# Performance work log

Hardware: AMD Instinct MI355X
Metric: run time of the kernel (lower is better)

Reference implementation:

```python
import jax, jax.numpy as jnp
import numpy as np

N = 20000   # nodes
E = 320000  # edges
T = 12      # sequence_length
H = 64      # hidden_dim
CIN = 16    # input_dim_per_step
L = 3       # num_st_layers
BN_EPS = 1e-5


def setup_inputs() -> dict:
    key = jax.random.key(0)
    ks = jax.random.split(key, 30)
    s = 0.05
    rn = lambda k, shp: jax.random.normal(k, shp, jnp.float32) * s
    inp = {
        "x": jax.random.normal(ks[0], (N, T * CIN), jnp.float32),
        "edge_index": jax.random.randint(ks[1], (2, E), 0, N, jnp.int32),
        # embedding
        "We": rn(ks[2], (CIN, H)), "be": rn(ks[3], (H,)),
        # stacked per-layer params for the 3 ST layers
        "gcn_W": rn(ks[4], (L, H, H)), "gcn_b": rn(ks[5], (L, H)),
        "conv_w": rn(ks[6], (L, H, H, 3)), "conv_b": rn(ks[7], (L, H)),
        "bn_g": jnp.ones((L, H), jnp.float32), "bn_b": rn(ks[8], (L, H)),
        "bn_m": rn(ks[9], (L, H)),
        "bn_v": jax.random.uniform(ks[10], (L, H), jnp.float32, 0.5, 1.5),
        # temporal attention MLP (H -> H//2 -> 1)
        "ta_w1": rn(ks[11], (H, H // 2)), "ta_b1": rn(ks[12], (H // 2,)),
        "ta_w2": rn(ks[13], (H // 2, 1)), "ta_b2": rn(ks[14], (1,)),
        # feature attention MLP (T -> T//2 -> 1)
        "fa_w1": rn(ks[15], (T, T // 2)), "fa_b1": rn(ks[16], (T // 2,)),
        "fa_w2": rn(ks[17], (T // 2, 1)), "fa_b2": rn(ks[18], (1,)),
        # output MLP (H -> H//2 -> 1)
        "ow1": rn(ks[19], (H, H // 2)), "ob1": rn(ks[20], (H // 2,)),
        "ow2": rn(ks[21], (H // 2, 1)), "ob2": rn(ks[22], (1,)),
    }
    return inp


def reference(x, edge_index, We, be, gcn_W, gcn_b, conv_w, conv_b,
              bn_g, bn_b, bn_m, bn_v, ta_w1, ta_b1, ta_w2, ta_b2,
              fa_w1, fa_b1, fa_w2, fa_b2, ow1, ob1, ow2, ob2):
    n = x.shape[0]
    # --- GCN normalization with self-loops (PyG gcn_norm) ---
    loops = jnp.arange(n, dtype=edge_index.dtype)
    src = jnp.concatenate([edge_index[0], loops])
    dst = jnp.concatenate([edge_index[1], loops])
    deg = jax.ops.segment_sum(jnp.ones_like(src, jnp.float32), dst, num_segments=n)
    dinv = 1.0 / jnp.sqrt(deg)  # deg >= 1 thanks to self-loops
    coef = dinv[src] * dinv[dst]  # [E+N]

    # --- per-timestep embedding (vectorized over t) ---
    xr = x.reshape(n, T, CIN)
    emb = jax.nn.relu(jnp.einsum('ntc,ch->nth', xr, We) + be)  # [N,T,H]
    x_st = emb.reshape(n, T * H)

    # --- ST layers (replicating original row-major .view layout mixing) ---
    for i in range(L):
        xi = x_st.reshape(n, H, T)  # [N,C,T]
        # GCNConv per timestep, batched over t: linear then normalized aggregate
        h = jnp.einsum('nct,cd->ndt', xi, gcn_W[i])          # [N,H,T]
        msg = coef[:, None, None] * h[src]                   # [E+N,H,T]
        agg = jax.ops.segment_sum(msg, dst, num_segments=n) + gcn_b[i][None, :, None]
        # temporal conv (kernel 3, pad 1) over T
        tmp = jax.lax.conv_general_dilated(
            agg, conv_w[i], (1,), [(1, 1)],
            dimension_numbers=('NCH', 'OIH', 'NCH')) + conv_b[i][None, :, None]
        # BatchNorm1d (eval mode: running stats)
        normed = (tmp - bn_m[i][None, :, None]) / jnp.sqrt(bn_v[i][None, :, None] + BN_EPS)
        normed = normed * bn_g[i][None, :, None] + bn_b[i][None, :, None]
        # residual is Identity (in_channels == out_channels)
        x_st = jax.nn.relu(normed + xi).reshape(n, H * T)

    # --- dual attention pooling ---
    xa = x_st.reshape(n, T, H)
    tw = (jnp.einsum('ntm,mk->ntk', jax.nn.relu(jnp.einsum('nth,hm->ntm', xa, ta_w1) + ta_b1), ta_w2) + ta_b2)[..., 0]
    tw = jax.nn.softmax(tw, axis=1)                          # [N,T]
    xt = (xa * tw[..., None]).transpose(0, 2, 1)             # [N,H,T]
    fw = (jnp.einsum('nhm,mk->nhk', jax.nn.relu(jnp.einsum('nht,tm->nhm', xt, fa_w1) + fa_b1), fa_w2) + fa_b2)[..., 0]
    fw = jax.nn.softmax(fw, axis=1)                          # [N,H]
    x_final = jnp.sum(xt * fw[..., None], axis=2)            # [N,H]

    # --- output MLP (dropout is identity in eval) ---
    out = jax.nn.relu(x_final @ ow1 + ob1) @ ow2 + ob2       # [N,1]
    return out
```

## Files before the change

### kernel.cpp

```cpp
#include <hip/hip_runtime.h>
#include <cstddef>
#include <cstdint>

#define T_ 12
#define H_ 64
#define CIN_ 16
#define F_ 768
#define BN_EPS 1e-5f
#define RPITCH 88
#define SLOTS 64

typedef float v2f __attribute__((ext_vector_type(2)));
typedef short s8v __attribute__((ext_vector_type(8)));
typedef float f4v __attribute__((ext_vector_type(4)));

__device__ __forceinline__ unsigned short f2bf(float f) {
    unsigned u = __float_as_uint(f);
    unsigned r = (u + 0x7FFFu + ((u >> 16) & 1u)) >> 16;
    return (unsigned short)r;
}
__device__ __forceinline__ float bf2f(unsigned short h) {
    return __uint_as_float(((unsigned)h) << 16);
}
__device__ __forceinline__ v2f bf2x2(unsigned u) {
    v2f r;
    r.x = __uint_as_float(u << 16);
    r.y = __uint_as_float(u & 0xFFFF0000u);
    return r;
}
__device__ __forceinline__ v2f pkfma(v2f a, v2f b, v2f c) {
    return __builtin_elementwise_fma(a, b, c);
}


__global__ void k_init(int* __restrict__ cursor, int n) {
    int i = blockIdx.x * 256 + threadIdx.x;
    if (i < n) cursor[i] = 0;
}


__global__ __launch_bounds__(256) void k_fused(
        const float* __restrict__ gcn_W, const float* __restrict__ gcn_b,
        const float* __restrict__ conv_w,
        unsigned short* __restrict__ wkA, float* __restrict__ bkp,
        const int* __restrict__ srcv, const int* __restrict__ dstv,
        int* __restrict__ cursor, int* __restrict__ csr_src, int e,
        const float* __restrict__ x, const float* __restrict__ We,
        const float* __restrict__ be, unsigned short* __restrict__ xbf, int nT,
        int nbE) {
    __shared__ float smem[5312];
    int b = blockIdx.x;
    int tid = threadIdx.x;

    if (b < 36) {
        int l = b / 12, k = (b / 4) % 3, cq = b & 3;
        const float* Wg = gcn_W + (size_t)l * 4096;
        const float* cw = conv_w + (size_t)l * 12288;
        float* scwT = smem;
        float* sWg  = smem + 4224;
        float* sgb  = smem + 5248;
        for (int i = tid; i < 4096; i += 256)
            scwT[(i & 63) * 66 + (i >> 6)] = cw[(size_t)i * 3 + k];
        for (int i = tid; i < 1024; i += 256)
            sWg[i] = Wg[cq * 16 * 64 + i];
        if (tid < 64) sgb[tid] = gcn_b[(size_t)l * 64 + tid];
        __syncthreads();
#pragma unroll
        for (int j = 0; j < 4; j++) {
            int idx = j * 256 + tid;
            int cc = idx >> 6;
            int o  = idx & 63;
            float acc = 0.f;
            for (int d = 0; d < 64; d++)
                acc += sWg[cc * 64 + d] * scwT[d * 66 + o];
            int cful = cq * 16 + cc;
            int kidx = k * 64 + cful;
            int ks = kidx >> 5, r = kidx & 31;
            int ln = (r >> 3) * 16 + (o & 15);
            int jj = r & 7;
            wkA[((((size_t)l * 24) + (o >> 4) * 6 + ks) * 64 + ln) * 8 + jj] =
                f2bf(acc);
        }
        if (cq == 0 && tid < 64) {
            int o = tid;
            float acc = 0.f;
            for (int d = 0; d < 64; d++)
                acc += sgb[d] * scwT[d * 66 + o];
            bkp[((size_t)l * 3 + k) * 64 + o] = acc;
        }
        return;
    }
    if (b < 36 + nbE) {
        int i = (b - 36) * 256 + tid;
        if (i < e) {
            int d = dstv[i], s = srcv[i];
            int pos = atomicAdd(&cursor[d], 1);
            if (pos < SLOTS) csr_src[d * SLOTS + pos] = s;
        }
        return;
    }
    float* sW = smem;
    float* sb = smem + 1024;
    for (int i = tid; i < CIN_ * H_; i += 256) sW[i] = We[i];
    if (tid < H_) sb[tid] = be[tid];
    __syncthreads();
    int h4  = tid & 15;
    int ntl = tid >> 4;
    int nt  = (b - 36 - nbE) * 16 + ntl;
    if (nt >= nT) return;
    const float4* xp = (const float4*)(x + (size_t)nt * CIN_);
    float4 xv4[4];
    xv4[0] = xp[0]; xv4[1] = xp[1]; xv4[2] = xp[2]; xv4[3] = xp[3];
    const float* xs = (const float*)xv4;
    float acc[4];
#pragma unroll
    for (int j = 0; j < 4; j++) acc[j] = sb[h4 * 4 + j];
#pragma unroll
    for (int c = 0; c < CIN_; c++) {
        float4 w = *(const float4*)&sW[c * H_ + h4 * 4];
        float xc = xs[c];
        acc[0] += xc * w.x; acc[1] += xc * w.y;
        acc[2] += xc * w.z; acc[3] += xc * w.w;
    }
    ushort4 h;
    h.x = f2bf(fmaxf(acc[0], 0.f)); h.y = f2bf(fmaxf(acc[1], 0.f));
    h.z = f2bf(fmaxf(acc[2], 0.f)); h.w = f2bf(fmaxf(acc[3], 0.f));
    *(ushort4*)&xbf[(size_t)nt * H_ + h4 * 4] = h;
}


__global__ __launch_bounds__(256) void k_post(
        const int* __restrict__ cursor, const int* __restrict__ csr_src,
        int2* __restrict__ pack, float* __restrict__ dinv, int n) {
    int i = blockIdx.x * 256 + threadIdx.x;
    int node = i >> 6, slot = i & 63;
    if (node >= n) return;
    int deg = cursor[node];
    float dn = rsqrtf((float)(deg + 1));
    if (slot == 0) dinv[node] = dn;
    if (slot < min(deg, SLOTS)) {
        int s = csr_src[node * SLOTS + slot];
        float cf = rsqrtf((float)(cursor[s] + 1)) * dn;
        pack[node * SLOTS + slot] = make_int2(s * 384, __float_as_int(cf));
    }
}


__global__ __launch_bounds__(256, 8) void k_gather(
        const unsigned short* __restrict__ xin,
        unsigned short* __restrict__ agg,
        const int* __restrict__ degv, const int2* __restrict__ pack,
        const float* __restrict__ dinv, int n) {
    __shared__ int2 sed[4 * SLOTS];
    int b = blockIdx.x;
    int sl = b & 7;
    int g = b >> 3;
    int wave = threadIdx.x >> 6, lane = threadIdx.x & 63;
    int node = g * 4 + wave;
    if (node >= n) return;
    int cnt = min(degv[node], SLOTS);
    if (lane < cnt) sed[wave * SLOTS + lane] = pack[node * SLOTS + lane];
    int lb = sl * 48 + (lane < 48 ? lane : 47);
    const unsigned* xu = (const unsigned*)xin;
    float dn = dinv[node];
    float cs = dn * dn;
    v2f cs2 = {cs, cs};
    v2f acc = bf2x2(xu[node * 384 + lb]) * cs2;
    const int2* sp = &sed[wave * SLOTS];
    int e = 0;
    for (; e + 3 < cnt; e += 4) {
        int2 p0 = sp[e], p1 = sp[e + 1], p2 = sp[e + 2], p3 = sp[e + 3];
        unsigned u0 = xu[p0.x + lb];
        unsigned u1 = xu[p1.x + lb];
        unsigned u2 = xu[p2.x + lb];
        unsigned u3 = xu[p3.x + lb];
        v2f c0 = {__int_as_float(p0.y), __int_as_float(p0.y)};
        v2f c1 = {__int_as_float(p1.y), __int_as_float(p1.y)};
        v2f c2 = {__int_as_float(p2.y), __int_as_float(p2.y)};
        v2f c3 = {__int_as_float(p3.y), __int_as_float(p3.y)};
        acc = pkfma(bf2x2(u0), c0, acc);
        acc = pkfma(bf2x2(u1), c1, acc);
        acc = pkfma(bf2x2(u2), c2, acc);
        acc = pkfma(bf2x2(u3), c3, acc);
    }
    for (; e < cnt; e++) {
        int2 p0 = sp[e];
        unsigned u0 = xu[p0.x + lb];
        v2f c0 = {__int_as_float(p0.y), __int_as_float(p0.y)};
        acc = pkfma(bf2x2(u0), c0, acc);
    }
    if (lane < 48) {
        unsigned o = (unsigned)f2bf(acc.x) | ((unsigned)f2bf(acc.y) << 16);
        ((unsigned*)agg)[node * 384 + lb] = o;
    }
}


#define CONV_CORE()                                                            \
    int tid = threadIdx.x;                                                     \
    int n0 = blockIdx.x * 8;                                                   \
    int wave = tid >> 6, lane = tid & 63;                                      \
    for (int i = tid; i < 8 * 2 * RPITCH; i += 256) {                          \
        int s = i / (2 * RPITCH);                                              \
        int r = i - s * (2 * RPITCH);                                          \
        int row = (r < RPITCH) ? 0 : 13;                                       \
        int c = (r < RPITCH) ? r : r - RPITCH;                                 \
        sxb[s * 14 * RPITCH + row * RPITCH + c] = 0;                           \
    }                                                                          \
    {                                                                          \
        int i0 = 3 * lane;                                                     \
        for (int si = 0; si < 2; si++) {                                       \
            int s = wave * 2 + si;                                             \
            int nn = n0 + s; if (nn >= n) nn = n - 1;                          \
            const uint2* ap = (const uint2*)(agg + (size_t)nn * F_);           \
            uint2 u0 = ap[i0], u1 = ap[i0 + 1], u2 = ap[i0 + 2];               \
            unsigned short* wp = &sxb[s * 14 * RPITCH + RPITCH + lane];        \
            wp[0]           = (unsigned short)u0.x;                            \
            wp[RPITCH]      = (unsigned short)(u0.x >> 16);                    \
            wp[2 * RPITCH]  = (unsigned short)u0.y;                            \
            wp[3 * RPITCH]  = (unsigned short)(u0.y >> 16);                    \
            wp[4 * RPITCH]  = (unsigned short)u1.x;                            \
            wp[5 * RPITCH]  = (unsigned short)(u1.x >> 16);                    \
            wp[6 * RPITCH]  = (unsigned short)u1.y;                            \
            wp[7 * RPITCH]  = (unsigned short)(u1.y >> 16);                    \
            wp[8 * RPITCH]  = (unsigned short)u2.x;                            \
            wp[9 * RPITCH]  = (unsigned short)(u2.x >> 16);                    \
            wp[10 * RPITCH] = (unsigned short)u2.y;                            \
            wp[11 * RPITCH] = (unsigned short)(u2.y >> 16);                    \
        }                                                                      \
    }                                                                          \
    __syncthreads();                                                           \
    int mt = wave;                                                             \
    int q = lane >> 4;                                                         \
    int l15 = lane & 15;                                                       \
    s8v afr[6];                                                                \
    const s8v* Ap = (const s8v*)wkA;                                           \
    for (int ks = 0; ks < 6; ks++) afr[ks] = Ap[(mt * 6 + ks) * 64 + lane];    \
    int obase = mt * 16 + q * 4;                                               \
    float scl[4], shf[4], ball[4], bk0a[4], bk2a[4];                           \
    for (int r = 0; r < 4; r++) {                                              \
        int o = obase + r;                                                     \
        float sc = bng[o] * rsqrtf(bnv[o] + BN_EPS);                           \
        scl[r] = sc;                                                           \
        shf[r] = bnb[o] - bnm[o] * sc;                                         \
        float b0 = bkp[o], b1 = bkp[64 + o], b2 = bkp[128 + o];                \
        ball[r] = cb[o] + b0 + b1 + b2;                                        \
        bk0a[r] = b0; bk2a[r] = b2;                                            \
    }                                                                          \
    f4v accv[6];                                                               \
    for (int nt = 0; nt < 6; nt++) {                                           \
        int nidx = nt * 16 + l15;                                              \
        int s = nidx / 12, t = nidx - 12 * s;                                  \
        const s8v* bp = (const s8v*)&sxb[s * 14 * RPITCH + t * RPITCH + q * 8];\
        f4v acc = {0.f, 0.f, 0.f, 0.f};                                        \
        acc = __builtin_amdgcn_mfma_f32_16x16x32_bf16(afr[0], bp[0],  acc, 0, 0, 0); \
        acc = __builtin_amdgcn_mfma_f32_16x16x32_bf16(afr[1], bp[4],  acc, 0, 0, 0); \
        acc = __builtin_amdgcn_mfma_f32_16x16x32_bf16(afr[2], bp[11], acc, 0, 0, 0); \
        acc = __builtin_amdgcn_mfma_f32_16x16x32_bf16(afr[3], bp[15], acc, 0, 0, 0); \
        acc = __builtin_amdgcn_mfma_f32_16x16x32_bf16(afr[4], bp[22], acc, 0, 0, 0); \
        acc = __builtin_amdgcn_mfma_f32_16x16x32_bf16(afr[5], bp[26], acc, 0, 0, 0); \
        accv[nt] = acc;                                                        \
    }                                                                          \
    __syncthreads();                                                           \
    for (int nt = 0; nt < 6; nt++) {                                           \
        int nidx = nt * 16 + l15;                                              \
        int s = nidx / 12, t = nidx - 12 * s;                                  \
        unsigned short* dp = &sxb[s * F_ + t];                                 \
        for (int r = 0; r < 4; r++) {                                          \
            float bias = ball[r];                                              \
            if (t == 0)  bias -= bk0a[r];                                      \
            if (t == 11) bias -= bk2a[r];                                      \
            float v = (accv[nt][r] + bias) * scl[r] + shf[r];                  \
            dp[(obase + r) * 12] = f2bf(v);                                    \
        }                                                                      \
    }                                                                          \
    __syncthreads();


__global__ __launch_bounds__(256, 8) void k_conv(
        const unsigned short* __restrict__ agg,
        const unsigned short* __restrict__ xin,
        unsigned short* __restrict__ xout,
        const unsigned short* __restrict__ wkA,
        const float* __restrict__ bkp, const float* __restrict__ cb,
        const float* __restrict__ bng, const float* __restrict__ bnb,
        const float* __restrict__ bnm, const float* __restrict__ bnv,
        int n) {
    __shared__ __align__(16) unsigned short sxb[8 * 14 * RPITCH];
    CONV_CORE()

#pragma unroll
    for (int cidx = 0; cidx < 3; cidx++) {
        int c = cidx * 256 + tid;
        int s = c / 96, off = c - s * 96;
        int nn = n0 + s;
        if (nn >= n) continue;
        uint4 dv = *(const uint4*)&sxb[s * F_ + off * 8];
        uint4 rv = ((const uint4*)(xin + (size_t)nn * F_))[off];
        uint4 ov;
        unsigned* dvp = (unsigned*)&dv;
        unsigned* rvp = (unsigned*)&rv;
        unsigned* ovp = (unsigned*)&ov;
#pragma unroll
        for (int w = 0; w < 4; w++) {
            v2f d2 = bf2x2(dvp[w]);
            v2f r2 = bf2x2(rvp[w]);
            float lo = fmaxf(d2.x + r2.x, 0.f);
            float hi = fmaxf(d2.y + r2.y, 0.f);
            ovp[w] = (unsigned)f2bf(lo) | ((unsigned)f2bf(hi) << 16);
        }
        *(uint4*)(xout + (size_t)nn * F_ + off * 8) = ov;
    }
}


__global__ __launch_bounds__(256, 7) void k_conv_attn(
        const unsigned short* __restrict__ agg,
        const unsigned short* __restrict__ xin,
        const unsigned short* __restrict__ wkA,
        const float* __restrict__ bkp, const float* __restrict__ cb,
        const float* __restrict__ bng, const float* __restrict__ bnb,
        const float* __restrict__ bnm, const float* __restrict__ bnv,
        const float* __restrict__ taw1, const float* __restrict__ tab1,
        const float* __restrict__ taw2, const float* __restrict__ tab2,
        const float* __restrict__ faw1, const float* __restrict__ fab1,
        const float* __restrict__ faw2, const float* __restrict__ fab2,
        const float* __restrict__ ow1, const float* __restrict__ ob1,
        const float* __restrict__ ow2, const float* __restrict__ ob2,
        float* __restrict__ out, int n) {
    __shared__ __align__(16) unsigned short sxb[8 * 14 * RPITCH];
    __shared__ float sft[96 + 520];
    CONV_CORE()

#pragma unroll
    for (int cidx = 0; cidx < 3; cidx++) {
        int c = cidx * 256 + tid;
        int s = c / 96, off = c - s * 96;
        int nn = n0 + s; if (nn >= n) nn = n - 1;
        uint4 dv = *(const uint4*)&sxb[s * F_ + off * 8];
        uint4 rv = ((const uint4*)(xin + (size_t)nn * F_))[off];
        unsigned* dvp = (unsigned*)&dv;
        unsigned* rvp = (unsigned*)&rv;
#pragma unroll
        for (int w = 0; w < 4; w++) {
            v2f d2 = bf2x2(dvp[w]);
            v2f r2 = bf2x2(rvp[w]);
            float lo = fmaxf(d2.x + r2.x, 0.f);
            float hi = fmaxf(d2.y + r2.y, 0.f);
            dvp[w] = (unsigned)f2bf(lo) | ((unsigned)f2bf(hi) << 16);
        }
        *(uint4*)&sxb[s * F_ + off * 8] = dv;
    }
    __syncthreads();

    float* s_tw = sft;
    float* s_xf = sft + 96;

    {
        int s2 = tid >> 5, m = tid & 31;
        float bm = tab1[m];
        v2f aa0 = {bm, bm}, aa1 = aa0, aa2 = aa0;
        v2f aa3 = aa0, aa4 = aa0, aa5 = aa0;
        const unsigned short* xr = &sxb[s2 * F_];
        float tb2 = tab2[0];
        for (int hh = 0; hh < 64; hh++) {
            const uint2* xp2 = (const uint2*)&xr[hh * 12];
            uint2 w0 = xp2[0], w1 = xp2[1], w2 = xp2[2];
            float wv = taw1[hh * 32 + m];
            v2f wv2 = {wv, wv};
            aa0 = pkfma(bf2x2(w0.x), wv2, aa0);
            aa1 = pkfma(bf2x2(w0.y), wv2, aa1);
            aa2 = pkfma(bf2x2(w1.x), wv2, aa2);
            aa3 = pkfma(bf2x2(w1.y), wv2, aa3);
            aa4 = pkfma(bf2x2(w2.x), wv2, aa4);
            aa5 = pkfma(bf2x2(w2.y), wv2, aa5);
        }
        float w2v = taw2[m];
        float av[12] = {aa0.x, aa0.y, aa1.x, aa1.y, aa2.x, aa2.y,
                        aa3.x, aa3.y, aa4.x, aa4.y, aa5.x, aa5.y};
#pragma unroll
        for (int t = 0; t < 12; t++) {
            float p = fmaxf(av[t], 0.f) * w2v;
            p += __shfl_xor(p, 1); p += __shfl_xor(p, 2);
            p += __shfl_xor(p, 4); p += __shfl_xor(p, 8);
            p += __shfl_xor(p, 16);
            if (m == 0) s_tw[s2 * 12 + t] = p + tb2;
        }
    }
    __syncthreads();

    {
        float fb2 = fab2[0];
        for (int qi = 0; qi < 2; qi++) {
            int ss = wave * 2 + qi;
            float tw[12];
#pragma unroll
            for (int t = 0; t < 12; t++) tw[t] = s_tw[ss * 12 + t];
            float mx = tw[0];
#pragma unroll
            for (int t = 1; t < 12; t++) mx = fmaxf(mx, tw[t]);
            float sum = 0.f;
#pragma unroll
            for (int t = 0; t < 12; t++) { tw[t] = __expf(tw[t] - mx); sum += tw[t]; }
            float inv = 1.f / sum;
            const uint2* xp2 = (const uint2*)&sxb[ss * F_ + lane * 12];
            uint2 w0 = xp2[0], w1 = xp2[1], w2 = xp2[2];
            v2f x0 = bf2x2(w0.x), x1 = bf2x2(w0.y), x2 = bf2x2(w1.x);
            v2f x3 = bf2x2(w1.y), x4 = bf2x2(w2.x), x5 = bf2x2(w2.y);
            float xv[12] = {x0.x, x0.y, x1.x, x1.y, x2.x, x2.y,
                            x3.x, x3.y, x4.x, x4.y, x5.x, x5.y};
            float xt[12];
#pragma unroll
            for (int t = 0; t < 12; t++) xt[t] = xv[t] * tw[t] * inv;
            float lf = fb2;
#pragma unroll
            for (int mm = 0; mm < 6; mm++) {
                float v = fab1[mm];
#pragma unroll
                for (int t = 0; t < 12; t++) v += xt[t] * faw1[t * 6 + mm];
                lf += fmaxf(v, 0.f) * faw2[mm];
            }
            float m2v = lf;
#pragma unroll
            for (int off = 32; off >= 1; off >>= 1)
                m2v = fmaxf(m2v, __shfl_xor(m2v, off));
            float ev = __expf(lf - m2v);
            float sev = ev;
#pragma unroll
            for (int off = 32; off >= 1; off >>= 1) sev += __shfl_xor(sev, off);
            float fwv = ev / sev;
            float xs = 0.f;
#pragma unroll
            for (int t = 0; t < 12; t++) xs += xt[t];
            s_xf[ss * 65 + lane] = fwv * xs;
        }
    }
    __syncthreads();

    {
        int s2 = tid >> 5, m = tid & 31;
        float v = ob1[m];
        const float* xfp = &s_xf[s2 * 65];
        for (int hh = 0; hh < 64; hh++) v += xfp[hh] * ow1[hh * 32 + m];
        float p = fmaxf(v, 0.f) * ow2[m];
        p += __shfl_xor(p, 1); p += __shfl_xor(p, 2);
        p += __shfl_xor(p, 4); p += __shfl_xor(p, 8);
        p += __shfl_xor(p, 16);
        if (m == 0 && n0 + s2 < n) out[n0 + s2] = p + ob2[0];
    }
}


extern "C" void kernel_launch(void* const* d_in, const int* in_sizes, int n_in,
                              void* d_out, int out_size, void* d_ws, size_t ws_size,
                              hipStream_t stream) {
    const float* x      = (const float*)d_in[0];
    const int*   ei     = (const int*)d_in[1];
    const float* We     = (const float*)d_in[2];
    const float* be     = (const float*)d_in[3];
    const float* gcn_W  = (const float*)d_in[4];
    const float* gcn_b  = (const float*)d_in[5];
    const float* conv_w = (const float*)d_in[6];
    const float* conv_b = (const float*)d_in[7];
    const float* bn_g   = (const float*)d_in[8];
    const float* bn_b   = (const float*)d_in[9];
    const float* bn_m   = (const float*)d_in[10];
    const float* bn_v   = (const float*)d_in[11];
    const float* ta_w1  = (const float*)d_in[12];
    const float* ta_b1  = (const float*)d_in[13];
    const float* ta_w2  = (const float*)d_in[14];
    const float* ta_b2  = (const float*)d_in[15];
    const float* fa_w1  = (const float*)d_in[16];
    const float* fa_b1  = (const float*)d_in[17];
    const float* fa_w2  = (const float*)d_in[18];
    const float* fa_b2  = (const float*)d_in[19];
    const float* ow1    = (const float*)d_in[20];
    const float* ob1    = (const float*)d_in[21];
    const float* ow2    = (const float*)d_in[22];
    const float* ob2    = (const float*)d_in[23];

    int n = in_sizes[0] / (T_ * CIN_);
    int e = in_sizes[1] / 2;
    const int* srcv = ei;
    const int* dstv = ei + e;

    char* p = (char*)d_ws;
    auto take = [&](size_t bytes) -> void* {
        void* r = (void*)p;
        p += (bytes + 255) & ~(size_t)255;
        return r;
    };
    int*   cursor    = (int*)take((size_t)n * 4);
    float* dinv      = (float*)take((size_t)n * 4);
    int*   csr_src   = (int*)take((size_t)n * SLOTS * 4);
    int2*  pack      = (int2*)take((size_t)n * SLOTS * 8);
    float* bkp       = (float*)take((size_t)3 * 3 * 64 * 4);
    unsigned short* wkA  = (unsigned short*)take((size_t)3 * 24 * 64 * 8 * 2);
    unsigned short* xabf = (unsigned short*)take((size_t)n * F_ * 2);
    unsigned short* xbbf = (unsigned short*)take((size_t)n * F_ * 2);
    unsigned short* aggb = (unsigned short*)take((size_t)n * F_ * 2);

    int nb_n = (n + 255) / 256;
    int nb_e = (e + 255) / 256;
    int nb8  = (n + 7) / 8;
    int nbG  = 8 * ((n + 3) / 4);
    int nT   = n * T_;
    int nbM  = (nT + 15) / 16;

    k_init<<<nb_n, 256, 0, stream>>>(cursor, n);
    k_fused<<<36 + nb_e + nbM, 256, 0, stream>>>(
        gcn_W, gcn_b, conv_w, wkA, bkp,
        srcv, dstv, cursor, csr_src, e,
        x, We, be, xabf, nT, nb_e);
    k_post<<<(n * SLOTS + 255) / 256, 256, 0, stream>>>(
        cursor, csr_src, pack, dinv, n);

    k_gather<<<nbG, 256, 0, stream>>>(xabf, aggb, cursor, pack, dinv, n);
    k_conv<<<nb8, 256, 0, stream>>>(aggb, xabf, xbbf, wkA, bkp, conv_b,
                                    bn_g, bn_b, bn_m, bn_v, n);
    k_gather<<<nbG, 256, 0, stream>>>(xbbf, aggb, cursor, pack, dinv, n);
    k_conv<<<nb8, 256, 0, stream>>>(aggb, xbbf, xabf,
                                    wkA + (size_t)1 * 24 * 64 * 8,
                                    bkp + (size_t)1 * 3 * 64,
                                    conv_b + (size_t)1 * H_,
                                    bn_g + (size_t)1 * H_, bn_b + (size_t)1 * H_,
                                    bn_m + (size_t)1 * H_, bn_v + (size_t)1 * H_,
                                    n);
    k_gather<<<nbG, 256, 0, stream>>>(xabf, aggb, cursor, pack, dinv, n);
    k_conv_attn<<<nb8, 256, 0, stream>>>(aggb, xabf,
                                         wkA + (size_t)2 * 24 * 64 * 8,
                                         bkp + (size_t)2 * 3 * 64,
                                         conv_b + (size_t)2 * H_,
                                         bn_g + (size_t)2 * H_, bn_b + (size_t)2 * H_,
                                         bn_m + (size_t)2 * H_, bn_v + (size_t)2 * H_,
                                         ta_w1, ta_b1, ta_w2, ta_b2,
                                         fa_w1, fa_b1, fa_w2, fa_b2,
                                         ow1, ob1, ow2, ob2, (float*)d_out, n);
}
```

Measured before the change: 495.0 us.

## Store node features in 8 feature-sliced planes for cache-local gathers

Changes the bf16 activation layout from node-major [N,768] to eight planes of [N,96], one per gather slice, so each k_gather block's random neighbour reads stay within a plane of about 3.8MB instead of spanning the whole 30MB array. The embedding writer, gather, conv input load and residual/output paths are all re-indexed to match the new layout. The gather also uses nontemporal loads for edge packs and nontemporal stores for the aggregate so they do not displace feature data in cache. The conv kernels now read and write with strided per-plane addressing, which costs some coalescing there.

```diff
diff --git a/kernel.cpp b/kernel.cpp
--- a/kernel.cpp
+++ b/kernel.cpp
@@ -9,6 +9,7 @@
 #define BN_EPS 1e-5f
 #define RPITCH 88
 #define SLOTS 64
+
 
 typedef float v2f __attribute__((ext_vector_type(2)));
 typedef short s8v __attribute__((ext_vector_type(8)));
@@ -47,7 +48,7 @@
         int* __restrict__ cursor, int* __restrict__ csr_src, int e,
         const float* __restrict__ x, const float* __restrict__ We,
         const float* __restrict__ be, unsigned short* __restrict__ xbf, int nT,
-        int nbE) {
+        int nbE, int n) {
     __shared__ float smem[5312];
     int b = blockIdx.x;
     int tid = threadIdx.x;
@@ -125,7 +126,10 @@
     ushort4 h;
     h.x = f2bf(fmaxf(acc[0], 0.f)); h.y = f2bf(fmaxf(acc[1], 0.f));
     h.z = f2bf(fmaxf(acc[2], 0.f)); h.w = f2bf(fmaxf(acc[3], 0.f));
-    *(ushort4*)&xbf[(size_t)nt * H_ + h4 * 4] = h;
+    int node = nt / 12, tt = nt - node * 12;
+    int flat = tt * 64 + h4 * 4;
+    int s = flat / 96, rem = flat - s * 96;
+    *(ushort4*)&xbf[((size_t)s * n + node) * 96 + rem] = h;
 }
 
 
@@ -141,7 +145,7 @@
     if (slot < min(deg, SLOTS)) {
         int s = csr_src[node * SLOTS + slot];
         float cf = rsqrtf((float)(cursor[s] + 1)) * dn;
-        pack[node * SLOTS + slot] = make_int2(s * 384, __float_as_int(cf));
+        pack[node * SLOTS + slot] = make_int2(s * 48, __float_as_int(cf));
     }
 }
 
@@ -159,13 +163,18 @@
     int node = g * 4 + wave;
     if (node >= n) return;
     int cnt = min(degv[node], SLOTS);
-    if (lane < cnt) sed[wave * SLOTS + lane] = pack[node * SLOTS + lane];
-    int lb = sl * 48 + (lane < 48 ? lane : 47);
-    const unsigned* xu = (const unsigned*)xin;
+    if (lane < cnt) {
+        long long v = __builtin_nontemporal_load(
+            (const long long*)&pack[node * SLOTS + lane]);
+        sed[wave * SLOTS + lane] = *(int2*)&v;
+    }
+    int planeU = sl * (n * 48);
+    const unsigned* xu = (const unsigned*)xin + planeU;
+    int lb = (lane < 48 ? lane : 47);
     float dn = dinv[node];
     float cs = dn * dn;
     v2f cs2 = {cs, cs};
-    v2f acc = bf2x2(xu[node * 384 + lb]) * cs2;
+    v2f acc = bf2x2(xu[node * 48 + lb]) * cs2;
     const int2* sp = &sed[wave * SLOTS];
     int e = 0;
     for (; e + 3 < cnt; e += 4) {
@@ -191,7 +200,8 @@
     }
     if (lane < 48) {
         unsigned o = (unsigned)f2bf(acc.x) | ((unsigned)f2bf(acc.y) << 16);
-        ((unsigned*)agg)[node * 384 + lb] = o;
+        unsigned* au = (unsigned*)agg + planeU;
+        __builtin_nontemporal_store(o, &au[node * 48 + lane]);
     }
 }
 
@@ -208,12 +218,13 @@
         sxb[s * 14 * RPITCH + row * RPITCH + c] = 0;                           \
     }                                                                          \
     {                                                                          \
-        int i0 = 3 * lane;                                                     \
+        const uint2* ab = (const uint2*)agg;                                   \
+        int pofs = (lane >> 3) * (n * 24) + (lane & 7) * 3;                    \
         for (int si = 0; si < 2; si++) {                                       \
             int s = wave * 2 + si;                                             \
             int nn = n0 + s; if (nn >= n) nn = n - 1;                          \
-            const uint2* ap = (const uint2*)(agg + (size_t)nn * F_);           \
-            uint2 u0 = ap[i0], u1 = ap[i0 + 1], u2 = ap[i0 + 2];               \
+            const uint2* ap = ab + pofs + nn * 24;                             \
+            uint2 u0 = ap[0], u1 = ap[1], u2 = ap[2];                          \
             unsigned short* wp = &sxb[s * 14 * RPITCH + RPITCH + lane];        \
             wp[0]           = (unsigned short)u0.x;                            \
             wp[RPITCH]      = (unsigned short)(u0.x >> 16);                    \
@@ -295,8 +306,10 @@
         int s = c / 96, off = c - s * 96;
         int nn = n0 + s;
         if (nn >= n) continue;
+        int sp = off / 12, rem = off - sp * 12;
+        int gidx = sp * (n * 12) + nn * 12 + rem;
         uint4 dv = *(const uint4*)&sxb[s * F_ + off * 8];
-        uint4 rv = ((const uint4*)(xin + (size_t)nn * F_))[off];
+        uint4 rv = ((const uint4*)xin)[gidx];
         uint4 ov;
         unsigned* dvp = (unsigned*)&dv;
         unsigned* rvp = (unsigned*)&rv;
@@ -309,7 +322,7 @@
             float hi = fmaxf(d2.y + r2.y, 0.f);
             ovp[w] = (unsigned)f2bf(lo) | ((unsigned)f2bf(hi) << 16);
         }
-        *(uint4*)(xout + (size_t)nn * F_ + off * 8) = ov;
+        ((uint4*)xout)[gidx] = ov;
     }
 }
 
@@ -337,8 +350,10 @@
         int c = cidx * 256 + tid;
         int s = c / 96, off = c - s * 96;
         int nn = n0 + s; if (nn >= n) nn = n - 1;
+        int sp = off / 12, rem = off - sp * 12;
+        int gidx = sp * (n * 12) + nn * 12 + rem;
         uint4 dv = *(const uint4*)&sxb[s * F_ + off * 8];
-        uint4 rv = ((const uint4*)(xin + (size_t)nn * F_))[off];
+        uint4 rv = ((const uint4*)xin)[gidx];
         unsigned* dvp = (unsigned*)&dv;
         unsigned* rvp = (unsigned*)&rv;
 #pragma unroll
@@ -511,7 +526,7 @@
     k_fused<<<36 + nb_e + nbM, 256, 0, stream>>>(
         gcn_W, gcn_b, conv_w, wkA, bkp,
         srcv, dstv, cursor, csr_src, e,
-        x, We, be, xabf, nT, nb_e);
+        x, We, be, xabf, nT, nb_e, n);
     k_post<<<(n * SLOTS + 255) / 256, 256, 0, stream>>>(
         cursor, csr_src, pack, dinv, n);
 
```

New measurement: 523.3 us. 5.7% more time.
